# Performance work log

Measured on AMD Instinct MI355X. Metric: run time of the kernel, lower is better.

Reference implementation:

```python
import jax, jax.numpy as jnp
import numpy as np

NEG_INF = -1e9


def setup_inputs() -> dict:
    key = jax.random.key(0)
    k1, k2, k3 = jax.random.split(key, 3)
    B, S, D, N, K = 8, 4096, 1024, 128, 8
    hidden_states = jax.random.normal(k1, (B, S, D), dtype=jnp.float32)
    sentence_indicator = jnp.sort(
        jax.random.randint(k2, (B, S), 0, N), axis=-1).astype(jnp.int64)
    cls_w = jax.random.normal(k3, (D,), dtype=jnp.float32) * (1.0 / np.sqrt(D))
    cls_b = jnp.zeros((), dtype=jnp.float32)
    return {
        "hidden_states": hidden_states,
        "sentence_indicator": sentence_indicator,
        "cls_w": cls_w,
        "cls_b": cls_b,
        "num_sentences": N,
        "extraction_k": K,
    }


def _selection_loop(hidden_states, sentence_indicator, cls_w, cls_b,
                    num_sentences, extraction_k):
    # --- sentence segment-sum pooling (replaces per-sentence masked-sum loop) ---
    seg_sum = jax.vmap(
        lambda h, ind: jax.ops.segment_sum(h, ind, num_segments=num_sentences)
    )(hidden_states, sentence_indicator)               # [B, N, D]
    counts = jax.vmap(
        lambda ind: jax.ops.segment_sum(
            jnp.ones(ind.shape, jnp.float32), ind, num_segments=num_sentences)
    )(sentence_indicator)                              # [B, N]
    sentence_lens = jnp.clip(counts, 1.0)[..., None]   # [B, N, 1], clamp(min=1)
    sentence_mask0 = (counts > 0).astype(jnp.float32)  # valid-sentence mask [B, N]

    B, N, D = seg_sum.shape

    def step(carry, _):
        cur_sum, cur_len, smask, sel = carry
        combined = cur_sum[:, None, :] + seg_sum           # [B, N, D]
        combined_len = cur_len[:, None, :] + sentence_lens  # [B, N, 1]
        pooled = combined / combined_len                    # [B, N, D]
        logits = jnp.einsum('bnd,d->bn', pooled, cls_w) + cls_b
        logits = jnp.where(smask > 0, logits, NEG_INF)      # mask_tensor
        idx = jnp.argmax(logits, axis=-1)                   # eval path (argmax)
        one_hot = jax.nn.one_hot(idx, N, dtype=jnp.float32)  # [B, N]
        smask = (1.0 - one_hot) * smask
        new_sum = jnp.einsum('bn,bnd->bd', one_hot, combined)
        new_len = jnp.sum(one_hot[..., None] * combined_len, axis=1)  # [B, 1]
        return (new_sum, new_len, smask, sel + one_hot), logits

    init = (jnp.zeros((B, D), jnp.float32),
            jnp.zeros((B, 1), jnp.float32),
            sentence_mask0,
            jnp.zeros((B, N), jnp.float32))
    (_, _, _, selected), all_logits = jax.lax.scan(
        step, init, None, length=extraction_k)
    selected = jnp.clip(selected, 0.0, 1.0)  # clamp(max=1)
    return selected, all_logits  # [B,N], [K,B,N]


def reference(hidden_states, sentence_indicator, cls_w, cls_b,
              num_sentences, extraction_k):
    selected_one_hot, all_logits = _selection_loop(
        hidden_states, sentence_indicator, cls_w, cls_b,
        num_sentences, extraction_k)
    # convert_attention_mask: token is kept iff its sentence was selected
    new_attention_mask = jnp.take_along_axis(
        selected_one_hot, sentence_indicator, axis=1)      # [B, S] float 0/1
    masked_hidden_states = new_attention_mask[..., None] * hidden_states
    return selected_one_hot, all_logits, new_attention_mask, masked_hidden_states
```

## Files before the change

### kernel.cpp

```cpp
#include <hip/hip_runtime.h>

#define B_ 8
#define S_ 4096
#define D_ 1024
#define N_ 128
#define K_ 8
#define NEG_INF_ (-1e9f)

__global__ void seg_dot_kernel(const float* __restrict__ h,
                               const int* __restrict__ ind,
                               const float* __restrict__ cls_w,
                               float* __restrict__ dot_seg,
                               float* __restrict__ counts) {
    const int bn = blockIdx.x;
    const int b = bn / N_;
    const int n = bn % N_;
    const int tid = threadIdx.x;
    const int* indb = ind + b * S_;

    int s0, s1;
    {
        int lo = 0, hi = S_;
        while (lo < hi) { int mid = (lo + hi) >> 1; if (indb[mid] < n) lo = mid + 1; else hi = mid; }
        s0 = lo;
        lo = s0; hi = S_;
        while (lo < hi) { int mid = (lo + hi) >> 1; if (indb[mid] < n + 1) lo = mid + 1; else hi = mid; }
        s1 = lo;
    }

    const int dofs = tid * 4;
    float4 acc = make_float4(0.f, 0.f, 0.f, 0.f);
    const float* hb = h + (size_t)b * S_ * D_;
    for (int s = s0; s < s1; ++s) {
        const float4 v = *reinterpret_cast<const float4*>(hb + (size_t)s * D_ + dofs);
        acc.x += v.x; acc.y += v.y; acc.z += v.z; acc.w += v.w;
    }
    const float4 w4 = *reinterpret_cast<const float4*>(cls_w + dofs);
    float partial = acc.x * w4.x + acc.y * w4.y + acc.z * w4.z + acc.w * w4.w;

    for (int off = 32; off > 0; off >>= 1) partial += __shfl_down(partial, off, 64);
    __shared__ float wsum[4];
    const int wv = tid >> 6, lane = tid & 63;
    if (lane == 0) wsum[wv] = partial;
    __syncthreads();
    if (tid == 0) {
        dot_seg[bn] = wsum[0] + wsum[1] + wsum[2] + wsum[3];
        counts[bn] = (float)(s1 - s0);
    }
}

__global__ void select_kernel(const float* __restrict__ dot_seg,
                              const float* __restrict__ counts,
                              const float* __restrict__ cls_b,
                              float* __restrict__ out_selected,
                              float* __restrict__ out_logits,
                              float* __restrict__ sel_ws) {
    const int b = blockIdx.x;
    const int tid = threadIdx.x;

    __shared__ float red_val[N_];
    __shared__ int   red_idx[N_];
    __shared__ float s_dotcur, s_lencur;

    const float dseg = dot_seg[b * N_ + tid];
    const float c    = counts[b * N_ + tid];
    const float len  = fmaxf(c, 1.0f);
    float smask = (c > 0.f) ? 1.f : 0.f;
    float sel   = 0.f;
    if (tid == 0) { s_dotcur = 0.f; s_lencur = 0.f; }
    const float bias = cls_b[0];
    __syncthreads();

    for (int k = 0; k < K_; ++k) {
        float logit = (s_dotcur + dseg) / (s_lencur + len) + bias;
        logit = (smask > 0.f) ? logit : NEG_INF_;
        out_logits[(size_t)k * (B_ * N_) + b * N_ + tid] = logit;
        red_val[tid] = logit;
        red_idx[tid] = tid;
        __syncthreads();
        for (int off = 64; off > 0; off >>= 1) {
            if (tid < off) {
                float v2 = red_val[tid + off]; int i2 = red_idx[tid + off];
                if (v2 > red_val[tid] || (v2 == red_val[tid] && i2 < red_idx[tid])) {
                    red_val[tid] = v2; red_idx[tid] = i2;
                }
            }
            __syncthreads();
        }
        const int pick = red_idx[0];
        if (tid == pick) { smask = 0.f; sel = 1.f; }
        if (tid == 0) {
            s_dotcur += red_val[0] != NEG_INF_ ? 0.f : 0.f;
        }
        __syncthreads();
        if (tid == pick) {
            s_dotcur += dseg;
            s_lencur += len;
        }
        __syncthreads();
    }

    out_selected[b * N_ + tid] = sel;
    sel_ws[b * N_ + tid] = sel;
}

__global__ void mask_kernel(const float* __restrict__ h,
                            const int* __restrict__ ind,
                            const float* __restrict__ sel_ws,
                            float* __restrict__ out_mask,
                            float* __restrict__ out_masked) {
    const int token = blockIdx.x;
    const int b = token >> 12;
    const int tid = threadIdx.x;
    const int id = ind[token];
    const float m = sel_ws[b * N_ + id];
    if (tid == 0) out_mask[token] = m;
    const size_t base = (size_t)token * D_ + tid * 4;
    if (m == 0.f) {
        *reinterpret_cast<float4*>(out_masked + base) = make_float4(0.f, 0.f, 0.f, 0.f);
    } else {
        const float4 v = *reinterpret_cast<const float4*>(h + base);
        *reinterpret_cast<float4*>(out_masked + base) =
            make_float4(v.x * m, v.y * m, v.z * m, v.w * m);
    }
}

extern "C" void kernel_launch(void* const* d_in, const int* in_sizes, int n_in,
                              void* d_out, int out_size, void* d_ws, size_t ws_size,
                              hipStream_t stream) {
    const float* h     = (const float*)d_in[0];
    const int*   ind   = (const int*)d_in[1];
    const float* cls_w = (const float*)d_in[2];
    const float* cls_b = (const float*)d_in[3];

    float* out = (float*)d_out;
    float* out_selected = out;
    float* out_logits   = out + 1024;
    float* out_mask     = out + 1024 + 8192;
    float* out_masked   = out + 1024 + 8192 + 32768;

    char* ws = (char*)d_ws;
    float* dot_seg = (float*)ws;
    float* cnts    = (float*)(ws + B_ * N_ * 4);
    float* sel_ws  = (float*)(ws + 2 * B_ * N_ * 4);

    seg_dot_kernel<<<dim3(B_ * N_), dim3(256), 0, stream>>>(h, ind, cls_w, dot_seg, cnts);
    select_kernel<<<dim3(B_), dim3(N_), 0, stream>>>(dot_seg, cnts, cls_b,
                                                     out_selected, out_logits, sel_ws);
    mask_kernel<<<dim3(B_ * S_), dim3(256), 0, stream>>>(h, ind, sel_ws, out_mask, out_masked);
}
```

Measured before the change: 59.77 us.

## Compute per-token dot products first, then segment-sum scalars in select kernel

Measured after the change: 58.44 us. -2.2%, faster.

```diff
diff --git a/kernel.cpp b/kernel.cpp
--- a/kernel.cpp
+++ b/kernel.cpp
@@ -7,50 +7,35 @@
 #define K_ 8
 #define NEG_INF_ (-1e9f)
 
-__global__ void seg_dot_kernel(const float* __restrict__ h,
-                               const int* __restrict__ ind,
+__global__ void tok_dot_kernel(const float* __restrict__ h,
                                const float* __restrict__ cls_w,
-                               float* __restrict__ dot_seg,
-                               float* __restrict__ counts) {
-    const int bn = blockIdx.x;
-    const int b = bn / N_;
-    const int n = bn % N_;
-    const int tid = threadIdx.x;
-    const int* indb = ind + b * S_;
+                               float* __restrict__ tok_dot) {
+    const int lane = threadIdx.x & 63;
+    const int gw = (blockIdx.x << 2) + (threadIdx.x >> 6);
+    const int dofs = lane * 4;
 
-    int s0, s1;
-    {
-        int lo = 0, hi = S_;
-        while (lo < hi) { int mid = (lo + hi) >> 1; if (indb[mid] < n) lo = mid + 1; else hi = mid; }
-        s0 = lo;
-        lo = s0; hi = S_;
-        while (lo < hi) { int mid = (lo + hi) >> 1; if (indb[mid] < n + 1) lo = mid + 1; else hi = mid; }
-        s1 = lo;
-    }
+    const float4 w0 = *reinterpret_cast<const float4*>(cls_w + 0 * 256 + dofs);
+    const float4 w1 = *reinterpret_cast<const float4*>(cls_w + 1 * 256 + dofs);
+    const float4 w2 = *reinterpret_cast<const float4*>(cls_w + 2 * 256 + dofs);
+    const float4 w3 = *reinterpret_cast<const float4*>(cls_w + 3 * 256 + dofs);
 
-    const int dofs = tid * 4;
-    float4 acc = make_float4(0.f, 0.f, 0.f, 0.f);
-    const float* hb = h + (size_t)b * S_ * D_;
-    for (int s = s0; s < s1; ++s) {
-        const float4 v = *reinterpret_cast<const float4*>(hb + (size_t)s * D_ + dofs);
-        acc.x += v.x; acc.y += v.y; acc.z += v.z; acc.w += v.w;
-    }
-    const float4 w4 = *reinterpret_cast<const float4*>(cls_w + dofs);
-    float partial = acc.x * w4.x + acc.y * w4.y + acc.z * w4.z + acc.w * w4.w;
-
-    for (int off = 32; off > 0; off >>= 1) partial += __shfl_down(partial, off, 64);
-    __shared__ float wsum[4];
-    const int wv = tid >> 6, lane = tid & 63;
-    if (lane == 0) wsum[wv] = partial;
-    __syncthreads();
-    if (tid == 0) {
-        dot_seg[bn] = wsum[0] + wsum[1] + wsum[2] + wsum[3];
-        counts[bn] = (float)(s1 - s0);
+    for (int token = gw; token < B_ * S_; token += 8192) {
+        const float* p = h + (size_t)token * D_;
+        const float4 v0 = *reinterpret_cast<const float4*>(p + 0 * 256 + dofs);
+        const float4 v1 = *reinterpret_cast<const float4*>(p + 1 * 256 + dofs);
+        const float4 v2 = *reinterpret_cast<const float4*>(p + 2 * 256 + dofs);
+        const float4 v3 = *reinterpret_cast<const float4*>(p + 3 * 256 + dofs);
+        float acc = v0.x * w0.x + v0.y * w0.y + v0.z * w0.z + v0.w * w0.w
+                  + v1.x * w1.x + v1.y * w1.y + v1.z * w1.z + v1.w * w1.w
+                  + v2.x * w2.x + v2.y * w2.y + v2.z * w2.z + v2.w * w2.w
+                  + v3.x * w3.x + v3.y * w3.y + v3.z * w3.z + v3.w * w3.w;
+        for (int off = 32; off > 0; off >>= 1) acc += __shfl_down(acc, off, 64);
+        if (lane == 0) tok_dot[token] = acc;
     }
 }
 
-__global__ void select_kernel(const float* __restrict__ dot_seg,
-                              const float* __restrict__ counts,
+__global__ void select_kernel(const float* __restrict__ tok_dot,
+                              const int* __restrict__ ind,
                               const float* __restrict__ cls_b,
                               float* __restrict__ out_selected,
                               float* __restrict__ out_logits,
@@ -58,25 +43,45 @@
     const int b = blockIdx.x;
     const int tid = threadIdx.x;
 
+    __shared__ float td[S_];
+    __shared__ int   si[S_];
     __shared__ float red_val[N_];
     __shared__ int   red_idx[N_];
     __shared__ float s_dotcur, s_lencur;
 
-    const float dseg = dot_seg[b * N_ + tid];
-    const float c    = counts[b * N_ + tid];
-    const float len  = fmaxf(c, 1.0f);
-    float smask = (c > 0.f) ? 1.f : 0.f;
-    float sel   = 0.f;
+    for (int s = tid; s < S_; s += 256) {
+        td[s] = tok_dot[b * S_ + s];
+        si[s] = ind[b * S_ + s];
+    }
     if (tid == 0) { s_dotcur = 0.f; s_lencur = 0.f; }
+    __syncthreads();
+
+    float dseg = 0.f, len = 1.f, smask = 0.f, sel = 0.f;
+    if (tid < N_) {
+        const int n = tid;
+        int lo = 0, hi = S_;
+        while (lo < hi) { int mid = (lo + hi) >> 1; if (si[mid] < n) lo = mid + 1; else hi = mid; }
+        const int s0 = lo;
+        lo = s0; hi = S_;
+        while (lo < hi) { int mid = (lo + hi) >> 1; if (si[mid] < n + 1) lo = mid + 1; else hi = mid; }
+        const int s1 = lo;
+        float acc = 0.f;
+        for (int s = s0; s < s1; ++s) acc += td[s];
+        dseg  = acc;
+        len   = fmaxf((float)(s1 - s0), 1.0f);
+        smask = (s1 > s0) ? 1.f : 0.f;
+    }
     const float bias = cls_b[0];
     __syncthreads();
 
     for (int k = 0; k < K_; ++k) {
-        float logit = (s_dotcur + dseg) / (s_lencur + len) + bias;
-        logit = (smask > 0.f) ? logit : NEG_INF_;
-        out_logits[(size_t)k * (B_ * N_) + b * N_ + tid] = logit;
-        red_val[tid] = logit;
-        red_idx[tid] = tid;
+        if (tid < N_) {
+            float logit = (s_dotcur + dseg) / (s_lencur + len) + bias;
+            logit = (smask > 0.f) ? logit : NEG_INF_;
+            out_logits[(size_t)k * (B_ * N_) + b * N_ + tid] = logit;
+            red_val[tid] = logit;
+            red_idx[tid] = tid;
+        }
         __syncthreads();
         for (int off = 64; off > 0; off >>= 1) {
             if (tid < off) {
@@ -88,20 +93,18 @@
             __syncthreads();
         }
         const int pick = red_idx[0];
-        if (tid == pick) { smask = 0.f; sel = 1.f; }
-        if (tid == 0) {
-            s_dotcur += red_val[0] != NEG_INF_ ? 0.f : 0.f;
-        }
-        __syncthreads();
         if (tid == pick) {
+            smask = 0.f; sel = 1.f;
             s_dotcur += dseg;
             s_lencur += len;
         }
         __syncthreads();
     }
 
-    out_selected[b * N_ + tid] = sel;
-    sel_ws[b * N_ + tid] = sel;
+    if (tid < N_) {
+        out_selected[b * N_ + tid] = sel;
+        sel_ws[b * N_ + tid] = sel;
+    }
 }
 
 __global__ void mask_kernel(const float* __restrict__ h,
@@ -109,19 +112,22 @@
                             const float* __restrict__ sel_ws,
                             float* __restrict__ out_mask,
                             float* __restrict__ out_masked) {
-    const int token = blockIdx.x;
-    const int b = token >> 12;
+    const int t0 = blockIdx.x << 2;
     const int tid = threadIdx.x;
-    const int id = ind[token];
-    const float m = sel_ws[b * N_ + id];
-    if (tid == 0) out_mask[token] = m;
-    const size_t base = (size_t)token * D_ + tid * 4;
-    if (m == 0.f) {
-        *reinterpret_cast<float4*>(out_masked + base) = make_float4(0.f, 0.f, 0.f, 0.f);
-    } else {
-        const float4 v = *reinterpret_cast<const float4*>(h + base);
-        *reinterpret_cast<float4*>(out_masked + base) =
-            make_float4(v.x * m, v.y * m, v.z * m, v.w * m);
+    #pragma unroll
+    for (int i = 0; i < 4; ++i) {
+        const int token = t0 + i;
+        const int b = token >> 12;
+        const float m = sel_ws[b * N_ + ind[token]];
+        if (tid == 0) out_mask[token] = m;
+        const size_t base = (size_t)token * D_ + tid * 4;
+        if (m == 0.f) {
+            *reinterpret_cast<float4*>(out_masked + base) = make_float4(0.f, 0.f, 0.f, 0.f);
+        } else {
+            const float4 v = *reinterpret_cast<const float4*>(h + base);
+            *reinterpret_cast<float4*>(out_masked + base) =
+                make_float4(v.x * m, v.y * m, v.z * m, v.w * m);
+        }
     }
 }
 
@@ -140,12 +146,11 @@
     float* out_masked   = out + 1024 + 8192 + 32768;
 
     char* ws = (char*)d_ws;
-    float* dot_seg = (float*)ws;
-    float* cnts    = (float*)(ws + B_ * N_ * 4);
-    float* sel_ws  = (float*)(ws + 2 * B_ * N_ * 4);
+    float* tok_dot = (float*)ws;
+    float* sel_ws  = (float*)(ws + (size_t)B_ * S_ * 4);
 
-    seg_dot_kernel<<<dim3(B_ * N_), dim3(256), 0, stream>>>(h, ind, cls_w, dot_seg, cnts);
-    select_kernel<<<dim3(B_), dim3(N_), 0, stream>>>(dot_seg, cnts, cls_b,
-                                                     out_selected, out_logits, sel_ws);
-    mask_kernel<<<dim3(B_ * S_), dim3(256), 0, stream>>>(h, ind, sel_ws, out_mask, out_masked);
+    tok_dot_kernel<<<dim3(2048), dim3(256), 0, stream>>>(h, cls_w, tok_dot);
+    select_kernel<<<dim3(B_), dim3(256), 0, stream>>>(tok_dot, ind, cls_b,
+                                                      out_selected, out_logits, sel_ws);
+    mask_kernel<<<dim3(B_ * S_ / 4), dim3(256), 0, stream>>>(h, ind, sel_ws, out_mask, out_masked);
 }
```
